# Optimization experiments

Measured on AMD Instinct MI355X. Metric: run time of the kernel, lower is better.

Reference implementation:

```python
import jax, jax.numpy as jnp
import numpy as np

N_NODES = 50000
N_EDGES = 1600000
BATCH = 1
CHANNELS = 32


def setup_inputs() -> dict:
    key = jax.random.key(0)
    k1, k2, k3, k4 = jax.random.split(key, 4)
    x = jax.random.normal(k1, (BATCH, CHANNELS, N_NODES), dtype=jnp.float32)
    W = jax.random.uniform(k2, (N_NODES,), dtype=jnp.float32)
    iInd = jax.random.randint(k3, (N_EDGES,), 0, N_NODES)
    jInd = jax.random.randint(k4, (N_EDGES,), 0, N_NODES)
    return {"x": x, "W": W, "iInd": iInd, "jInd": jInd, "nnodes": N_NODES}


def reference(x, W, iInd, jInd, nnodes):
    # neighborNode: gather source-node features along edges, weighted by W[iInd]
    # (branch: W.shape[0] == x.shape[2] == nnodes)
    Wi = W[iInd]                      # [E]
    g = Wi * x[:, :, jInd]            # [B, C, E]
    # neighborEdge: scatter-add W[iInd] * g back to target nodes iInd
    # (branch: W.shape[0] == nnodes != E)
    out = jnp.zeros((x.shape[0], x.shape[1], nnodes), dtype=x.dtype)
    out = out.at[:, :, iInd].add(Wi * g)  # [B, C, nnodes]
    return out
```

## Files before the change

kernel.cpp:

```cpp
#include <hip/hip_runtime.h>
#include <math.h>


#define TCH 32
#define BSHIFT 7
#define BNODES 128
#define MAXNB 512
#define SLOTS 32
#define BIN_THREADS 512
#define TILE 4096
#define SR_THREADS 512
#define SPLIT2 4
#define NSUB 32
#define CMP_CAP 1536
#define SJ_CAP 1536

__device__ __forceinline__ unsigned short f32_to_bf16(float f) {
    unsigned int u = __float_as_uint(f);
    unsigned int r = (u + 0x7FFFu + ((u >> 16) & 1u)) >> 16;
    return (unsigned short)r;
}

__global__ void transpose_CN_to_NC_bf16(const float* __restrict__ x,
                                        unsigned short* __restrict__ xtb,
                                        int* __restrict__ gcursor,
                                        int NB, int N) {
    __shared__ float tile[32][33];
    const int tx = threadIdx.x;
    const int ty = threadIdx.y;
    if (blockIdx.x == 0) {
        const int flat = ty * 32 + tx;
        for (int k = flat; k < NB + 1; k += 1024) gcursor[k] = 0;
    }
    const int n0 = blockIdx.x * 32;
    const int n = n0 + tx;
    if (n < N) tile[ty][tx] = x[(size_t)ty * N + n];
    __syncthreads();
    const int nw = n0 + ty;
    if (nw < N) xtb[(size_t)nw * TCH + tx] = f32_to_bf16(tile[tx][ty]);
}

__device__ __forceinline__ void push_ovf(int* ovf_cnt, int2* ovf, int ovf_cap,
                                         int i, int j) {
    const int p = atomicAdd(ovf_cnt, 1);
    if (p < ovf_cap) ovf[p] = make_int2(i, j);
}

__global__ __launch_bounds__(BIN_THREADS) void bin_edges(
    const int* __restrict__ iInd, const int* __restrict__ jInd,
    int* __restrict__ bins, int* __restrict__ gcursor,
    int* __restrict__ ovf_cnt, int2* __restrict__ ovf, int ovf_cap,
    int E, int NB, int cap) {
    __shared__ int stage[MAXNB * SLOTS];
    __shared__ int scnt[MAXNB];
    __shared__ int wsum[8];
    __shared__ unsigned short excl[MAXNB];
    __shared__ unsigned short gbase[MAXNB];
    __shared__ unsigned short bidx[TILE];
    const int tid = threadIdx.x;

    scnt[tid] = 0;
    __syncthreads();

    const int base = blockIdx.x * TILE + tid * 8;
#pragma unroll
    for (int q = 0; q < 2; ++q) {
        const int eb = base + q * 4;
        if (eb + 3 < E) {
            const int4 iv = *(const int4*)(iInd + eb);
            const int4 jv = *(const int4*)(jInd + eb);
            const int is[4] = {iv.x, iv.y, iv.z, iv.w};
            const int js[4] = {jv.x, jv.y, jv.z, jv.w};
#pragma unroll
            for (int k = 0; k < 4; ++k) {
                const int i = is[k], j = js[k];
                const int b = i >> BSHIFT;
                const int slot = atomicAdd(&scnt[b], 1);
                if (slot < SLOTS)
                    stage[b * SLOTS + slot] = ((i & (BNODES - 1)) << 16) | j;
                else
                    push_ovf(ovf_cnt, ovf, ovf_cap, i, j);
            }
        } else {
            for (int k = 0; k < 4; ++k) {
                const int e = eb + k;
                if (e < E) {
                    const int i = iInd[e], j = jInd[e];
                    const int b = i >> BSHIFT;
                    const int slot = atomicAdd(&scnt[b], 1);
                    if (slot < SLOTS)
                        stage[b * SLOTS + slot] = ((i & (BNODES - 1)) << 16) | j;
                    else
                        push_ovf(ovf_cnt, ovf, ovf_cap, i, j);
                }
            }
        }
    }
    __syncthreads();

    const int cb = min(scnt[tid], SLOTS);
    const int lane = tid & 63;
    const int wv = tid >> 6;
    int v = cb;
#pragma unroll
    for (int off = 1; off < 64; off <<= 1) {
        const int u = __shfl_up(v, off);
        if (lane >= off) v += u;
    }
    if (lane == 63) wsum[wv] = v;
    __syncthreads();
    if (tid < 8) {
        int s = wsum[tid];
#pragma unroll
        for (int off = 1; off < 8; off <<= 1) {
            const int u = __shfl_up(s, off, 8);
            if (tid >= off) s += u;
        }
        wsum[tid] = s;
    }
    __syncthreads();
    const int incl = v + (wv == 0 ? 0 : wsum[wv - 1]);
    const int run0 = incl - cb;
    const int total = wsum[7];
    excl[tid] = (unsigned short)run0;
    if (cb > 0) {
        gbase[tid] = (unsigned short)atomicAdd(&gcursor[tid], cb);
        for (int t = 0; t < cb; ++t)
            bidx[run0 + t] = (unsigned short)tid;
    }
    __syncthreads();

    for (int idx = tid; idx < total; idx += BIN_THREADS) {
        const int b = bidx[idx];
        const int k = idx - (int)excl[b];
        const int rec = stage[b * SLOTS + k];
        const int gslot = (int)gbase[b] + k;
        if (gslot < cap) {
            bins[(size_t)b * cap + gslot] = rec;
        } else {
            push_ovf(ovf_cnt, ovf, ovf_cap,
                     (b << BSHIFT) | (rec >> 16), rec & 0xFFFF);
        }
    }
}

__global__ __launch_bounds__(SR_THREADS) void sort_reduce5(
    const int* __restrict__ bins, const int* __restrict__ gcursor,
    const unsigned short* __restrict__ xtb, const float* __restrict__ W,
    float* __restrict__ out, int* __restrict__ ovf_cnt,
    int2* __restrict__ ovf, int ovf_cap, int N, int cap) {
    const int bucket = blockIdx.x >> 2;
    const int sub = blockIdx.x & (SPLIT2 - 1);
    __shared__ unsigned int cmp[CMP_CAP];
    __shared__ unsigned short sj[SJ_CAP];
    __shared__ float acc[NSUB * 33];
    __shared__ int hcnt[NSUB];
    __shared__ int off2[NSUB + 1];
    __shared__ int cur[NSUB];
    __shared__ int ccnt;

    int cnt = gcursor[bucket];
    if (cnt > cap) cnt = cap;
    const int* rec = bins + (size_t)bucket * cap;

    if (threadIdx.x < NSUB) { hcnt[threadIdx.x] = 0; cur[threadIdx.x] = 0; }
    if (threadIdx.x == 0) ccnt = 0;
    __syncthreads();

    const int cnt4 = cnt >> 2;
    const int4* rec4 = (const int4*)rec;
    for (int r = threadIdx.x; r < cnt4; r += SR_THREADS) {
        const int4 v = rec4[r];
        const unsigned int prs[4] = {(unsigned int)v.x, (unsigned int)v.y,
                                     (unsigned int)v.z, (unsigned int)v.w};
#pragma unroll
        for (int k = 0; k < 4; ++k) {
            const unsigned int pr = prs[k];
            const int il = (int)(pr >> 16);
            if ((il >> 5) == sub) {
                const int p = atomicAdd(&ccnt, 1);
                if (p < CMP_CAP) {
                    cmp[p] = pr;
                    atomicAdd(&hcnt[il & (NSUB - 1)], 1);
                } else {
                    push_ovf(ovf_cnt, ovf, ovf_cap,
                             (bucket << BSHIFT) | il, (int)(pr & 0xFFFF));
                }
            }
        }
    }
    for (int r = (cnt4 << 2) + threadIdx.x; r < cnt; r += SR_THREADS) {
        const unsigned int pr = (unsigned int)rec[r];
        const int il = (int)(pr >> 16);
        if ((il >> 5) == sub) {
            const int p = atomicAdd(&ccnt, 1);
            if (p < CMP_CAP) {
                cmp[p] = pr;
                atomicAdd(&hcnt[il & (NSUB - 1)], 1);
            } else {
                push_ovf(ovf_cnt, ovf, ovf_cap,
                         (bucket << BSHIFT) | il, (int)(pr & 0xFFFF));
            }
        }
    }
    __syncthreads();

    if (threadIdx.x == 0) {
        int run = 0;
        for (int k = 0; k < NSUB; ++k) { off2[k] = run; run += hcnt[k]; }
        off2[NSUB] = run;
    }
    __syncthreads();

    const int cc = min(ccnt, CMP_CAP);
    for (int r = threadIdx.x; r < cc; r += SR_THREADS) {
        const unsigned int pr = cmp[r];
        const int il = (int)(pr >> 16) & (NSUB - 1);
        const int pos = off2[il] + atomicAdd(&cur[il], 1);
        sj[pos] = (unsigned short)(pr & 0xFFFF);
    }
    __syncthreads();

    const int lane = threadIdx.x & 31;
    const int g = threadIdx.x >> 5;
    const int rslot = lane >> 3;
    const int c4 = (lane & 7) * 4;
    for (int ill = g; ill < NSUB; ill += SR_THREADS / 32) {
        const int beg = off2[ill];
        const int end = off2[ill + 1];
        float a0 = 0.f, a1 = 0.f, a2 = 0.f, a3 = 0.f;
        int rb = beg;
        for (; rb + 8 <= end; rb += 8) {
            const int j0 = sj[rb + rslot];
            const int j1 = sj[rb + 4 + rslot];
            const uint2 u0 = *(const uint2*)(xtb + (size_t)j0 * TCH + c4);
            const uint2 u1 = *(const uint2*)(xtb + (size_t)j1 * TCH + c4);
            a0 += __uint_as_float(u0.x << 16);
            a1 += __uint_as_float(u0.x & 0xFFFF0000u);
            a2 += __uint_as_float(u0.y << 16);
            a3 += __uint_as_float(u0.y & 0xFFFF0000u);
            a0 += __uint_as_float(u1.x << 16);
            a1 += __uint_as_float(u1.x & 0xFFFF0000u);
            a2 += __uint_as_float(u1.y << 16);
            a3 += __uint_as_float(u1.y & 0xFFFF0000u);
        }
        {
            const int rr = rb + rslot;
            if (rr < end) {
                const int j = sj[rr];
                const uint2 u = *(const uint2*)(xtb + (size_t)j * TCH + c4);
                a0 += __uint_as_float(u.x << 16);
                a1 += __uint_as_float(u.x & 0xFFFF0000u);
                a2 += __uint_as_float(u.y << 16);
                a3 += __uint_as_float(u.y & 0xFFFF0000u);
            }
            const int rr2 = rb + 4 + rslot;
            if (rr2 < end) {
                const int j = sj[rr2];
                const uint2 u = *(const uint2*)(xtb + (size_t)j * TCH + c4);
                a0 += __uint_as_float(u.x << 16);
                a1 += __uint_as_float(u.x & 0xFFFF0000u);
                a2 += __uint_as_float(u.y << 16);
                a3 += __uint_as_float(u.y & 0xFFFF0000u);
            }
        }
        a0 += __shfl_xor(a0, 8);  a1 += __shfl_xor(a1, 8);
        a2 += __shfl_xor(a2, 8);  a3 += __shfl_xor(a3, 8);
        a0 += __shfl_xor(a0, 16); a1 += __shfl_xor(a1, 16);
        a2 += __shfl_xor(a2, 16); a3 += __shfl_xor(a3, 16);
        if (rslot == 0) {
            float* ap = &acc[ill * 33 + c4];
            ap[0] = a0; ap[1] = a1; ap[2] = a2; ap[3] = a3;
        }
    }
    __syncthreads();

    const int i0 = (bucket << BSHIFT) + sub * NSUB;
    for (int k = threadIdx.x; k < NSUB * TCH; k += SR_THREADS) {
        const int ill = k & (NSUB - 1);
        const int cc2 = k >> 5;
        const int i = i0 + ill;
        if (i < N) {
            const float w = W[i];
            out[(size_t)cc2 * N + i] = w * w * acc[ill * 33 + cc2];
        }
    }
}

__global__ void overflow_apply(const int2* __restrict__ ovf,
                               const int* __restrict__ ovf_cnt,
                               const float* __restrict__ W,
                               const float* __restrict__ x,
                               float* __restrict__ out, int N, int ovf_cap) {
    int cnt = *ovf_cnt;
    if (cnt > ovf_cap) cnt = ovf_cap;
    const long long total = (long long)cnt * TCH;
    const long long stride = (long long)gridDim.x * blockDim.x;
    for (long long t = (long long)blockIdx.x * blockDim.x + threadIdx.x;
         t < total; t += stride) {
        const int e = (int)(t >> 5);
        const int c = (int)(t & 31);
        const int2 p = ovf[e];
        const float w = W[p.x];
        atomicAdd(&out[(size_t)c * N + p.x], w * w * x[(size_t)c * N + p.y]);
    }
}

__global__ void edge_scatter_cn(const int* __restrict__ iInd,
                                const int* __restrict__ jInd,
                                const float* __restrict__ W,
                                const float* __restrict__ x,
                                float* __restrict__ out, int E, int N) {
    const long long t = (long long)blockIdx.x * blockDim.x + threadIdx.x;
    const int e = (int)(t >> 5);
    const int c = (int)(t & 31);
    if (e < E) {
        const int i = iInd[e];
        const int j = jInd[e];
        const float w = W[i];
        atomicAdd(&out[(size_t)c * N + i], w * w * x[(size_t)c * N + j]);
    }
}

extern "C" void kernel_launch(void* const* d_in, const int* in_sizes, int n_in,
                              void* d_out, int out_size, void* d_ws, size_t ws_size,
                              hipStream_t stream) {
    const float* x    = (const float*)d_in[0];
    const float* W    = (const float*)d_in[1];
    const int*   iInd = (const int*)d_in[2];
    const int*   jInd = (const int*)d_in[3];

    const int N = in_sizes[1];
    const int E = in_sizes[2];
    float* out = (float*)d_out;

    const int NB = (N + BNODES - 1) >> BSHIFT;
    const int mean = (NB > 0) ? (E / NB) : 0;
    int cap = mean + (int)(8.0 * sqrt((double)(mean > 0 ? mean : 1))) + 64;
    cap = (cap + 3) & ~3;

    const size_t A = 256;
    const size_t xtb_bytes = (((size_t)N * TCH * 2) + A - 1) / A * A;
    const size_t bin_bytes = (((size_t)NB * cap * 4) + A - 1) / A * A;
    const size_t cur_bytes = (((size_t)(NB + 1) * 4) + A - 1) / A * A;
    const size_t base_need = xtb_bytes + bin_bytes + cur_bytes;

    int ovf_cap = 0;
    if (ws_size > base_need) {
        size_t avail = ws_size - base_need;
        size_t oc = avail / sizeof(int2);
        if (oc > (size_t)(1 << 21)) oc = (size_t)(1 << 21);
        ovf_cap = (int)oc;
    }

    if (ws_size >= base_need && ovf_cap >= 65536 && NB <= MAXNB &&
        N <= 65536 && cap < 60000) {
        char* wsb = (char*)d_ws;
        unsigned short* xtb = (unsigned short*)wsb;
        int*   bins    = (int*)(wsb + xtb_bytes);
        int*   gcursor = (int*)(wsb + xtb_bytes + bin_bytes);
        int*   ovf_cnt = gcursor + NB;
        int2*  ovf     = (int2*)(wsb + base_need);

        const int ntiles = (N + 31) / 32;
        dim3 tb(32, 32);
        transpose_CN_to_NC_bf16<<<ntiles, tb, 0, stream>>>(
            x, xtb, gcursor, NB, N);

        const int bin_blocks = (E + TILE - 1) / TILE;
        bin_edges<<<bin_blocks, BIN_THREADS, 0, stream>>>(
            iInd, jInd, bins, gcursor, ovf_cnt, ovf, ovf_cap, E, NB, cap);

        sort_reduce5<<<NB * SPLIT2, SR_THREADS, 0, stream>>>(
            bins, gcursor, xtb, W, out, ovf_cnt, ovf, ovf_cap, N, cap);

        overflow_apply<<<128, 256, 0, stream>>>(
            ovf, ovf_cnt, W, x, out, N, ovf_cap);
    } else {
        hipMemsetAsync(out, 0, (size_t)out_size * sizeof(float), stream);
        const int threads = 256;
        const long long total = (long long)E * TCH;
        const int blocks = (int)((total + threads - 1) / threads);
        edge_scatter_cn<<<blocks, threads, 0, stream>>>(iInd, jInd, W, x, out, E, N);
    }
}
```

Baseline: 51.45 us.

## Fuse transpose into binning kernel and fold overflow handling into reduce

The bf16 transpose now runs as extra blocks of the binning kernel, and counter initialization moves to a tiny separate kernel. The separate overflow kernel is removed: each reduce block scans the overflow list and applies only the entries that fall in its own node range. The compact buffer grows so the per-bucket cap always fits, which lets the reduce drop its overflow branch. Together these cut one launch and a dependency stage, at the cost of more shared memory per reduce block and every block scanning the whole overflow list.

```diff
diff --git a/kernel.cpp b/kernel.cpp
--- a/kernel.cpp
+++ b/kernel.cpp
@@ -12,8 +12,8 @@
 #define SR_THREADS 512
 #define SPLIT2 4
 #define NSUB 32
-#define CMP_CAP 1536
-#define SJ_CAP 1536
+#define CMP_CAP 4736
+#define SJ_CAP 4736
 
 __device__ __forceinline__ unsigned short f32_to_bf16(float f) {
     unsigned int u = __float_as_uint(f);
@@ -21,23 +21,8 @@
     return (unsigned short)r;
 }
 
-__global__ void transpose_CN_to_NC_bf16(const float* __restrict__ x,
-                                        unsigned short* __restrict__ xtb,
-                                        int* __restrict__ gcursor,
-                                        int NB, int N) {
-    __shared__ float tile[32][33];
-    const int tx = threadIdx.x;
-    const int ty = threadIdx.y;
-    if (blockIdx.x == 0) {
-        const int flat = ty * 32 + tx;
-        for (int k = flat; k < NB + 1; k += 1024) gcursor[k] = 0;
-    }
-    const int n0 = blockIdx.x * 32;
-    const int n = n0 + tx;
-    if (n < N) tile[ty][tx] = x[(size_t)ty * N + n];
-    __syncthreads();
-    const int nw = n0 + ty;
-    if (nw < N) xtb[(size_t)nw * TCH + tx] = f32_to_bf16(tile[tx][ty]);
+__global__ void init_counters(int* __restrict__ gcursor, int NB) {
+    for (int k = threadIdx.x; k < NB + 1; k += blockDim.x) gcursor[k] = 0;
 }
 
 __device__ __forceinline__ void push_ovf(int* ovf_cnt, int2* ovf, int ovf_cap,
@@ -46,11 +31,12 @@
     if (p < ovf_cap) ovf[p] = make_int2(i, j);
 }
 
-__global__ __launch_bounds__(BIN_THREADS) void bin_edges(
+__global__ __launch_bounds__(BIN_THREADS) void bin_and_transpose(
+    const float* __restrict__ x, unsigned short* __restrict__ xtb,
     const int* __restrict__ iInd, const int* __restrict__ jInd,
     int* __restrict__ bins, int* __restrict__ gcursor,
     int* __restrict__ ovf_cnt, int2* __restrict__ ovf, int ovf_cap,
-    int E, int NB, int cap) {
+    int E, int NB, int cap, int N, int binB) {
     __shared__ int stage[MAXNB * SLOTS];
     __shared__ int scnt[MAXNB];
     __shared__ int wsum[8];
@@ -58,6 +44,28 @@
     __shared__ unsigned short gbase[MAXNB];
     __shared__ unsigned short bidx[TILE];
     const int tid = threadIdx.x;
+
+    if (blockIdx.x >= binB) {
+        float* tilef = (float*)stage;
+        const int t = blockIdx.x - binB;
+        const int n0 = t * 32;
+        const int tx = tid & 31;
+        const int ty2 = tid >> 5;
+#pragma unroll
+        for (int h = 0; h < 32; h += 16) {
+            const int c = ty2 + h;
+            const int n = n0 + tx;
+            if (n < N) tilef[c * 33 + tx] = x[(size_t)c * N + n];
+        }
+        __syncthreads();
+#pragma unroll
+        for (int h = 0; h < 32; h += 16) {
+            const int ny = ty2 + h;
+            const int nw = n0 + ny;
+            if (nw < N) xtb[(size_t)nw * TCH + tx] = f32_to_bf16(tilef[tx * 33 + ny]);
+        }
+        return;
+    }
 
     scnt[tid] = 0;
     __syncthreads();
@@ -144,11 +152,12 @@
     }
 }
 
-__global__ __launch_bounds__(SR_THREADS) void sort_reduce5(
+__global__ __launch_bounds__(SR_THREADS) void sort_reduce7(
     const int* __restrict__ bins, const int* __restrict__ gcursor,
     const unsigned short* __restrict__ xtb, const float* __restrict__ W,
-    float* __restrict__ out, int* __restrict__ ovf_cnt,
-    int2* __restrict__ ovf, int ovf_cap, int N, int cap) {
+    const float* __restrict__ x, float* __restrict__ out,
+    const int* __restrict__ ovf_cnt, const int2* __restrict__ ovf,
+    int ovf_cap, int N, int cap) {
     const int bucket = blockIdx.x >> 2;
     const int sub = blockIdx.x & (SPLIT2 - 1);
     __shared__ unsigned int cmp[CMP_CAP];
@@ -179,13 +188,8 @@
             const int il = (int)(pr >> 16);
             if ((il >> 5) == sub) {
                 const int p = atomicAdd(&ccnt, 1);
-                if (p < CMP_CAP) {
-                    cmp[p] = pr;
-                    atomicAdd(&hcnt[il & (NSUB - 1)], 1);
-                } else {
-                    push_ovf(ovf_cnt, ovf, ovf_cap,
-                             (bucket << BSHIFT) | il, (int)(pr & 0xFFFF));
-                }
+                cmp[p] = pr;
+                atomicAdd(&hcnt[il & (NSUB - 1)], 1);
             }
         }
     }
@@ -194,13 +198,8 @@
         const int il = (int)(pr >> 16);
         if ((il >> 5) == sub) {
             const int p = atomicAdd(&ccnt, 1);
-            if (p < CMP_CAP) {
-                cmp[p] = pr;
-                atomicAdd(&hcnt[il & (NSUB - 1)], 1);
-            } else {
-                push_ovf(ovf_cnt, ovf, ovf_cap,
-                         (bucket << BSHIFT) | il, (int)(pr & 0xFFFF));
-            }
+            cmp[p] = pr;
+            atomicAdd(&hcnt[il & (NSUB - 1)], 1);
         }
     }
     __syncthreads();
@@ -212,7 +211,7 @@
     }
     __syncthreads();
 
-    const int cc = min(ccnt, CMP_CAP);
+    const int cc = ccnt;
     for (int r = threadIdx.x; r < cc; r += SR_THREADS) {
         const unsigned int pr = cmp[r];
         const int il = (int)(pr >> 16) & (NSUB - 1);
@@ -285,24 +284,19 @@
             out[(size_t)cc2 * N + i] = w * w * acc[ill * 33 + cc2];
         }
     }
-}
-
-__global__ void overflow_apply(const int2* __restrict__ ovf,
-                               const int* __restrict__ ovf_cnt,
-                               const float* __restrict__ W,
-                               const float* __restrict__ x,
-                               float* __restrict__ out, int N, int ovf_cap) {
-    int cnt = *ovf_cnt;
-    if (cnt > ovf_cap) cnt = ovf_cap;
-    const long long total = (long long)cnt * TCH;
-    const long long stride = (long long)gridDim.x * blockDim.x;
-    for (long long t = (long long)blockIdx.x * blockDim.x + threadIdx.x;
-         t < total; t += stride) {
-        const int e = (int)(t >> 5);
-        const int c = (int)(t & 31);
+    __syncthreads();
+
+    int ocnt = *ovf_cnt;
+    if (ocnt > ovf_cap) ocnt = ovf_cap;
+    for (int e = threadIdx.x; e < ocnt; e += SR_THREADS) {
         const int2 p = ovf[e];
-        const float w = W[p.x];
-        atomicAdd(&out[(size_t)c * N + p.x], w * w * x[(size_t)c * N + p.y]);
+        if (p.x >= i0 && p.x < i0 + NSUB) {
+            const float w = W[p.x];
+            const float w2 = w * w;
+            for (int c = 0; c < TCH; ++c)
+                atomicAdd(&out[(size_t)c * N + p.x],
+                          w2 * x[(size_t)c * N + p.y]);
+        }
     }
 }
 
@@ -354,7 +348,7 @@
     }
 
     if (ws_size >= base_need && ovf_cap >= 65536 && NB <= MAXNB &&
-        N <= 65536 && cap < 60000) {
+        N <= 65536 && cap <= CMP_CAP) {
         char* wsb = (char*)d_ws;
         unsigned short* xtb = (unsigned short*)wsb;
         int*   bins    = (int*)(wsb + xtb_bytes);
@@ -362,20 +356,16 @@
         int*   ovf_cnt = gcursor + NB;
         int2*  ovf     = (int2*)(wsb + base_need);
 
+        init_counters<<<1, 512, 0, stream>>>(gcursor, NB);
+
+        const int binB = (E + TILE - 1) / TILE;
         const int ntiles = (N + 31) / 32;
-        dim3 tb(32, 32);
-        transpose_CN_to_NC_bf16<<<ntiles, tb, 0, stream>>>(
-            x, xtb, gcursor, NB, N);
-
-        const int bin_blocks = (E + TILE - 1) / TILE;
-        bin_edges<<<bin_blocks, BIN_THREADS, 0, stream>>>(
-            iInd, jInd, bins, gcursor, ovf_cnt, ovf, ovf_cap, E, NB, cap);
-
-        sort_reduce5<<<NB * SPLIT2, SR_THREADS, 0, stream>>>(
-            bins, gcursor, xtb, W, out, ovf_cnt, ovf, ovf_cap, N, cap);
-
-        overflow_apply<<<128, 256, 0, stream>>>(
-            ovf, ovf_cnt, W, x, out, N, ovf_cap);
+        bin_and_transpose<<<binB + ntiles, BIN_THREADS, 0, stream>>>(
+            x, xtb, iInd, jInd, bins, gcursor, ovf_cnt, ovf, ovf_cap,
+            E, NB, cap, N, binB);
+
+        sort_reduce7<<<NB * SPLIT2, SR_THREADS, 0, stream>>>(
+            bins, gcursor, xtb, W, x, out, ovf_cnt, ovf, ovf_cap, N, cap);
     } else {
         hipMemsetAsync(out, 0, (size_t)out_size * sizeof(float), stream);
         const int threads = 256;
```

Result: faster. 49.54 us, median of 2 (-3.7%).
